# Kernel tuning notes

Measured on AMD Instinct MI355X. Metric: run time of the kernel, lower is better.

Reference implementation:

```python
import jax, jax.numpy as jnp
import numpy as np

D = 256; NH = 8; NL = 4; NP = 4; HD = D // NH
SHAPES = np.array([[64, 64], [32, 32], [16, 16], [8, 8]], dtype=np.int32)  # (H, W) per level
LSI = np.array([0, 4096, 5120, 5376], dtype=np.int32)
B = 4; LQ = int(SHAPES.prod(axis=1).sum())  # 5440


def setup_inputs() -> dict:
    key = jax.random.key(0)
    ks = jax.random.split(key, 16)
    p = lambda i, shape, s=0.02: jax.random.normal(ks[i], shape, dtype=jnp.float32) * s
    return dict(
        src=jax.random.normal(ks[0], (B, LQ, D), dtype=jnp.float32),
        pos=jax.random.normal(ks[1], (B, LQ, D), dtype=jnp.float32),
        reference_points=jax.random.uniform(ks[2], (B, LQ, NL, 2), dtype=jnp.float32),
        spatial_shapes=jnp.asarray(SHAPES),
        level_start_index=jnp.asarray(LSI),
        Wv=p(3, (D, D)), bv=jnp.zeros((D,), jnp.float32),
        Woff=p(4, (D, NH * NL * NP * 2)), boff=p(5, (NH * NL * NP * 2,)),
        Wattn=p(6, (D, NH * NL * NP)), battn=p(7, (NH * NL * NP,)),
        Wout=p(8, (D, D)), bout=jnp.zeros((D,), jnp.float32),
        g1=jnp.ones((D,), jnp.float32), b1=jnp.zeros((D,), jnp.float32),
        W1=p(9, (D, D)), bb1=jnp.zeros((D,), jnp.float32),
        W2=p(10, (D, D)), bb2=jnp.zeros((D,), jnp.float32),
        g3=jnp.ones((D,), jnp.float32), b3=jnp.zeros((D,), jnp.float32),
    )


def _ln(x, g, b, eps=1e-5):
    m = jnp.mean(x, -1, keepdims=True)
    v = jnp.mean(jnp.square(x - m), -1, keepdims=True)
    return (x - m) * jax.lax.rsqrt(v + eps) * g + b


def _bilinear(vflat, Hl, Wl, loc):
    # vflat: [B, Hl*Wl, nh, hd]; loc: [B, Lq, nh, np, 2] normalized to [0,1]
    # align_corners=False, zero padding (matches F.grid_sample in MSDeformAttn)
    x = loc[..., 0] * Wl - 0.5
    y = loc[..., 1] * Hl - 0.5
    x0 = jnp.floor(x); y0 = jnp.floor(y)
    fx = x - x0; fy = y - y0
    x0 = x0.astype(jnp.int32); y0 = y0.astype(jnp.int32)
    Bb, Lq, nh, npnt = x0.shape
    hd = vflat.shape[-1]
    out = jnp.zeros((Bb, Lq, nh, npnt, hd), vflat.dtype)
    for dy in (0, 1):
        for dx in (0, 1):
            xi = x0 + dx; yi = y0 + dy
            w = (fx if dx else 1.0 - fx) * (fy if dy else 1.0 - fy)
            valid = (xi >= 0) & (xi < Wl) & (yi >= 0) & (yi < Hl)
            idx = jnp.clip(yi, 0, Hl - 1) * Wl + jnp.clip(xi, 0, Wl - 1)  # [B,Lq,nh,np]
            idx = idx.transpose(0, 1, 3, 2).reshape(Bb, Lq * npnt, nh, 1)
            g = jnp.take_along_axis(vflat, idx, axis=1)
            g = g.reshape(Bb, Lq, npnt, nh, hd).transpose(0, 1, 3, 2, 4)
            out = out + g * (w * valid.astype(w.dtype))[..., None]
    return out  # [B, Lq, nh, np, hd]


def _forward(src, pos, reference_points, spatial_shapes, level_start_index,
             Wv, bv, Woff, boff, Wattn, battn, Wout, bout,
             g1, b1, W1, bb1, W2, bb2, g3, b3):
    shapes = np.asarray(spatial_shapes)
    lsi = np.asarray(level_start_index)
    Bq, Lq, Dm = src.shape
    q = src + pos  # with_pos_embed
    value = (src @ Wv + bv).reshape(Bq, Lq, NH, HD)
    off = (q @ Woff + boff).reshape(Bq, Lq, NH, NL, NP, 2)
    aw = jax.nn.softmax((q @ Wattn + battn).reshape(Bq, Lq, NH, NL * NP), axis=-1)
    aw = aw.reshape(Bq, Lq, NH, NL, NP)
    # offset normalizer is (W, H) per level
    norm = jnp.stack([shapes[:, 1].astype(np.float32), shapes[:, 0].astype(np.float32)], axis=-1)
    loc = reference_points[:, :, None, :, None, :] + off / norm[None, None, None, :, None, :]
    attended = jnp.zeros((Bq, Lq, NH, HD), src.dtype)
    for l in range(shapes.shape[0]):
        Hl, Wl = int(shapes[l, 0]), int(shapes[l, 1])
        s = int(lsi[l])
        vflat = value[:, s:s + Hl * Wl]
        sampled = _bilinear(vflat, Hl, Wl, loc[:, :, :, l])  # [B,Lq,nh,np,hd]
        attended = attended + jnp.einsum('blhpd,blhp->blhd', sampled, aw[:, :, :, l])
    src2 = attended.reshape(Bq, Lq, Dm) @ Wout + bout
    # residual + LayerNorm (dropout is identity in eval)
    sxy = _ln(src + src2, g1, b1)
    # FFN (d_ffn == d_model here), residual + LayerNorm
    h = jax.nn.relu(sxy @ W1 + bb1)
    return _ln(sxy + (h @ W2 + bb2), g3, b3)


def reference(src, pos, reference_points, spatial_shapes, level_start_index,
              Wv, bv, Woff, boff, Wattn, battn, Wout, bout,
              g1, b1, W1, bb1, W2, bb2, g3, b3):
    return _forward(src, pos, reference_points, spatial_shapes, level_start_index,
                    Wv, bv, Woff, boff, Wattn, battn, Wout, bout,
                    g1, b1, W1, bb1, W2, bb2, g3, b3)
```

## Files before the change

kernel.cpp:

```cpp
#include <hip/hip_runtime.h>
#include <cstddef>
#include <cstdint>

#define M_TOK 21760
#define LQ_ 5440

typedef _Float16 f16x8 __attribute__((ext_vector_type(8)));
typedef _Float16 h2v __attribute__((ext_vector_type(2)));
typedef float f32x4v __attribute__((ext_vector_type(4)));
typedef _Float16 half4v __attribute__((ext_vector_type(4)));

__device__ __forceinline__ unsigned short f2h(float f) {
  return __builtin_bit_cast(unsigned short, (_Float16)f);
}
__device__ __forceinline__ float h2f(unsigned short u) {
  return (float)__builtin_bit_cast(_Float16, u);
}

__global__ __launch_bounds__(256) void prep_k(
    const float* __restrict__ src, const float* __restrict__ pos,
    const float* __restrict__ Wv, const float* __restrict__ Woff,
    const float* __restrict__ Wattn, const float* __restrict__ Wout,
    const float* __restrict__ W1, const float* __restrict__ W2,
    unsigned short* __restrict__ s16, unsigned short* __restrict__ q16,
    unsigned short* __restrict__ G)
{
  const int b = blockIdx.x;
  if (b < 5440) {
    const int i = b * 256 + threadIdx.x;
    const float4 s = ((const float4*)src)[i];
    const float4 p = ((const float4*)pos)[i];
    ushort4 a, q;
    a.x = f2h(s.x); a.y = f2h(s.y); a.z = f2h(s.z); a.w = f2h(s.w);
    q.x = f2h(s.x + p.x); q.y = f2h(s.y + p.y); q.z = f2h(s.z + p.z); q.w = f2h(s.w + p.w);
    ((ushort4*)s16)[i] = a;
    ((ushort4*)q16)[i] = q;
  } else {
    const int gid = (b - 5440) * 256 + threadIdx.x;
    const float* srcs[6] = {Wv, Woff, Wattn, Wout, W1, W2};
    const int starts[7] = {0, 65536, 131072, 163840, 229376, 294912, 360448};
    const int Nn[6] = {256, 256, 128, 256, 256, 256};
    int m = 0;
#pragma unroll
    for (int i = 1; i < 6; ++i) m += (gid >= starts[i]);
    const int local = gid - starts[m];
    const int n = local >> 8;
    const int k = local & 255;
    G[gid] = f2h(srcs[m][(size_t)k * Nn[m] + n]);
  }
}

__global__ __launch_bounds__(256, 2) void gemm_qkv_k(
    const unsigned short* __restrict__ s16, const unsigned short* __restrict__ q16,
    const unsigned short* __restrict__ WvT, const unsigned short* __restrict__ WfT,
    const float* __restrict__ bv, const float* __restrict__ boff,
    const float* __restrict__ battn,
    unsigned short* __restrict__ value16, unsigned short* __restrict__ fused16)
{
  const int id = blockIdx.x;
  const int xcd = id & 7;
  const int local = id >> 3;
  const int sid = xcd * 106 + min(xcd, 2) + local;
  const int bx = sid / 5;
  const int by = sid % 5;

  const bool isv = (by < 2);
  const unsigned short* A  = isv ? s16 : q16;
  const unsigned short* Wt = isv ? WvT : WfT;
  const int n0 = isv ? by * 128 : (by - 2) * 128;
  const int N  = isv ? 256 : 384;
  unsigned short* out16 = isv ? value16 : fused16;
  const float* bsel; int nsub;
  if (isv)            { bsel = bv;    nsub = 0; }
  else if (n0 < 256)  { bsel = boff;  nsub = 0; }
  else                { bsel = battn; nsub = 256; }

  __shared__ unsigned short As[128 * 64];
  __shared__ unsigned short Bs[128 * 64];
  const int t = threadIdx.x;
  const int lane = t & 63, wave = t >> 6;
  const int wm = wave >> 1, wn = wave & 1;
  const int m0 = bx * 128;

  const int lrow = lane >> 3;
  const int pcol = (lane & 7) << 4;
  const int scol = pcol ^ (lrow << 4);

  f32x4v acc[4][4];
#pragma unroll
  for (int i = 0; i < 4; ++i)
#pragma unroll
    for (int j = 0; j < 4; ++j) acc[i][j] = (f32x4v){0.f, 0.f, 0.f, 0.f};

  const int fr = lane & 15;
  const int fkb = (lane >> 4) << 4;

  for (int k0 = 0; k0 < 256; k0 += 64) {
#pragma unroll
    for (int i = 0; i < 4; ++i) {
      const int row = wave * 32 + i * 8 + lrow;
      const unsigned short* g = A + (size_t)(m0 + row) * 256 + k0 + (scol >> 1);
      unsigned short* s = As + (wave * 32 + i * 8) * 64;
      __builtin_amdgcn_global_load_lds(
          (const __attribute__((address_space(1))) void*)g,
          (__attribute__((address_space(3))) void*)s, 16, 0, 0);
    }
#pragma unroll
    for (int i = 0; i < 4; ++i) {
      const int row = wave * 32 + i * 8 + lrow;
      const unsigned short* g = Wt + (size_t)(n0 + row) * 256 + k0 + (scol >> 1);
      unsigned short* s = Bs + (wave * 32 + i * 8) * 64;
      __builtin_amdgcn_global_load_lds(
          (const __attribute__((address_space(1))) void*)g,
          (__attribute__((address_space(3))) void*)s, 16, 0, 0);
    }
    __syncthreads();

    f16x8 af[4][2], bfr[4][2];
#pragma unroll
    for (int i = 0; i < 4; ++i) {
      const int row = wm * 64 + i * 16 + fr;
      const char* base = (const char*)As + row * 128;
#pragma unroll
      for (int kk = 0; kk < 2; ++kk)
        af[i][kk] = *(const f16x8*)(base + ((kk * 64 + fkb) ^ ((row & 7) << 4)));
    }
#pragma unroll
    for (int j = 0; j < 4; ++j) {
      const int row = wn * 64 + j * 16 + fr;
      const char* base = (const char*)Bs + row * 128;
#pragma unroll
      for (int kk = 0; kk < 2; ++kk)
        bfr[j][kk] = *(const f16x8*)(base + ((kk * 64 + fkb) ^ ((row & 7) << 4)));
    }
#pragma unroll
    for (int i = 0; i < 4; ++i)
#pragma unroll
      for (int j = 0; j < 4; ++j) {
        acc[i][j] = __builtin_amdgcn_mfma_f32_16x16x32_f16(af[i][0], bfr[j][0], acc[i][j], 0, 0, 0);
        acc[i][j] = __builtin_amdgcn_mfma_f32_16x16x32_f16(af[i][1], bfr[j][1], acc[i][j], 0, 0, 0);
      }
    __syncthreads();
  }

  const int fq = lane >> 4;
#pragma unroll
  for (int j = 0; j < 4; ++j) {
    const int n = n0 + wn * 64 + j * 16 + fr;
    const float bj = bsel[n - nsub];
#pragma unroll
    for (int i = 0; i < 4; ++i) {
#pragma unroll
      for (int r = 0; r < 4; ++r) {
        const int m = m0 + wm * 64 + i * 16 + fq * 4 + r;
        out16[(size_t)m * N + n] = f2h(acc[i][j][r] + bj);
      }
    }
  }
}

__global__ __launch_bounds__(512, 4) void gemm_ln_k(
    const unsigned short* __restrict__ A, const unsigned short* __restrict__ Wt,
    const float* __restrict__ bias, const float* __restrict__ resf,
    const unsigned short* __restrict__ res16,
    const float* __restrict__ g, const float* __restrict__ b,
    float* __restrict__ outf, unsigned short* __restrict__ out16)
{
  __shared__ unsigned short As[32 * 64];
  __shared__ unsigned short Bs[256 * 64 + 288];
  const int t = threadIdx.x;
  const int lane = t & 63, wave = t >> 6;
  const int rt = wave & 1, cg = wave >> 1;
  const int m0 = blockIdx.x * 32;

  const int lrow = lane >> 3;
  const int pcol = (lane & 7) << 4;
  const int scol = pcol ^ (lrow << 4);

  f32x4v acc[4];
#pragma unroll
  for (int j = 0; j < 4; ++j) acc[j] = (f32x4v){0.f, 0.f, 0.f, 0.f};

  const int fr = lane & 15;
  const int fq = lane >> 4;
  const int fkb = fq << 4;

  for (int k0 = 0; k0 < 256; k0 += 64) {
    if (wave < 4) {
      const int row = wave * 8 + lrow;
      const unsigned short* gp = A + (size_t)(m0 + row) * 256 + k0 + (scol >> 1);
      unsigned short* s = As + (wave * 8) * 64;
      __builtin_amdgcn_global_load_lds(
          (const __attribute__((address_space(1))) void*)gp,
          (__attribute__((address_space(3))) void*)s, 16, 0, 0);
    }
#pragma unroll
    for (int i = 0; i < 4; ++i) {
      const int row = wave * 32 + i * 8 + lrow;
      const unsigned short* gp = Wt + (size_t)row * 256 + k0 + (scol >> 1);
      unsigned short* s = Bs + (wave * 32 + i * 8) * 64;
      __builtin_amdgcn_global_load_lds(
          (const __attribute__((address_space(1))) void*)gp,
          (__attribute__((address_space(3))) void*)s, 16, 0, 0);
    }
    __syncthreads();

    f16x8 af0, af1;
    {
      const int arow = rt * 16 + fr;
      const char* abase = (const char*)As + arow * 128;
      af0 = *(const f16x8*)(abase + ((0 + fkb) ^ ((arow & 7) << 4)));
      af1 = *(const f16x8*)(abase + ((64 + fkb) ^ ((arow & 7) << 4)));
    }
#pragma unroll
    for (int j = 0; j < 4; ++j) {
      const int brow = cg * 64 + j * 16 + fr;
      const char* bbase = (const char*)Bs + brow * 128;
      const f16x8 b0 = *(const f16x8*)(bbase + ((0 + fkb) ^ ((brow & 7) << 4)));
      const f16x8 b1 = *(const f16x8*)(bbase + ((64 + fkb) ^ ((brow & 7) << 4)));
      acc[j] = __builtin_amdgcn_mfma_f32_16x16x32_f16(af0, b0, acc[j], 0, 0, 0);
      acc[j] = __builtin_amdgcn_mfma_f32_16x16x32_f16(af1, b1, acc[j], 0, 0, 0);
    }
    __syncthreads();
  }

  float* Cs = (float*)Bs;
#pragma unroll
  for (int j = 0; j < 4; ++j) {
    const int col = cg * 64 + j * 16 + fr;
#pragma unroll
    for (int rr = 0; rr < 4; ++rr) {
      const int row = rt * 16 + fq * 4 + rr;
      Cs[row * 260 + col] = acc[j][rr];
    }
  }
  __syncthreads();

  const int lg = lane >> 4, li = lane & 15;
  const int row = wave * 4 + lg;
  const size_t rowoff = (size_t)(m0 + row) * 256;

  float4 v[4];
  float s = 0.f;
#pragma unroll
  for (int c4 = 0; c4 < 4; ++c4) {
    const int col = c4 * 64 + li * 4;
    float4 x = *(float4*)&Cs[row * 260 + col];
    const float4 bi = *(const float4*)&bias[col];
    float4 rv;
    if (resf) {
      rv = *(const float4*)&resf[rowoff + col];
    } else {
      const ushort4 r16 = *(const ushort4*)&res16[rowoff + col];
      rv.x = h2f(r16.x); rv.y = h2f(r16.y); rv.z = h2f(r16.z); rv.w = h2f(r16.w);
    }
    x.x += bi.x + rv.x; x.y += bi.y + rv.y;
    x.z += bi.z + rv.z; x.w += bi.w + rv.w;
    v[c4] = x;
    s += x.x + x.y + x.z + x.w;
  }
#pragma unroll
  for (int o = 1; o < 16; o <<= 1) s += __shfl_xor(s, o);
  const float mean = s * (1.f / 256.f);
  float ss = 0.f;
#pragma unroll
  for (int c4 = 0; c4 < 4; ++c4) {
    const float d0 = v[c4].x - mean, d1 = v[c4].y - mean;
    const float d2 = v[c4].z - mean, d3 = v[c4].w - mean;
    ss += d0 * d0 + d1 * d1 + d2 * d2 + d3 * d3;
  }
#pragma unroll
  for (int o = 1; o < 16; o <<= 1) ss += __shfl_xor(ss, o);
  const float rstd = rsqrtf(ss * (1.f / 256.f) + 1e-5f);

#pragma unroll
  for (int c4 = 0; c4 < 4; ++c4) {
    const int col = c4 * 64 + li * 4;
    const float4 gv = *(const float4*)&g[col];
    const float4 bv = *(const float4*)&b[col];
    float4 o4;
    o4.x = (v[c4].x - mean) * rstd * gv.x + bv.x;
    o4.y = (v[c4].y - mean) * rstd * gv.y + bv.y;
    o4.z = (v[c4].z - mean) * rstd * gv.z + bv.z;
    o4.w = (v[c4].w - mean) * rstd * gv.w + bv.w;
    if (outf) *(float4*)(outf + rowoff + col) = o4;
    if (out16) {
      ushort4 o;
      o.x = f2h(o4.x); o.y = f2h(o4.y); o.z = f2h(o4.z); o.w = f2h(o4.w);
      *(ushort4*)(out16 + rowoff + col) = o;
    }
  }
}

__global__ __launch_bounds__(512, 4) void gemm_ffn_ln_k(
    const unsigned short* __restrict__ sxy16,
    const unsigned short* __restrict__ W1T, const unsigned short* __restrict__ W2T,
    const float* __restrict__ bb1, const float* __restrict__ bb2,
    const float* __restrict__ g, const float* __restrict__ b,
    float* __restrict__ outf)
{
  __shared__ unsigned short Bs[256 * 64 + 288];
  __shared__ unsigned short Hs[32 * 264];
  const int t = threadIdx.x;
  const int lane = t & 63, wave = t >> 6;
  const int rt = wave & 1, cg = wave >> 1;
  const int m0 = blockIdx.x * 32;

  const int lrow = lane >> 3;
  const int pcol = (lane & 7) << 4;
  const int scol = pcol ^ (lrow << 4);

  const int fr = lane & 15;
  const int fq = lane >> 4;
  const int fkb = fq << 4;

  f32x4v acc[4];
#pragma unroll
  for (int j = 0; j < 4; ++j) acc[j] = (f32x4v){0.f, 0.f, 0.f, 0.f};

  for (int k0 = 0; k0 < 256; k0 += 64) {
#pragma unroll
    for (int i = 0; i < 4; ++i) {
      const int row = wave * 32 + i * 8 + lrow;
      const unsigned short* gp = W1T + (size_t)row * 256 + k0 + (scol >> 1);
      unsigned short* s = Bs + (wave * 32 + i * 8) * 64;
      __builtin_amdgcn_global_load_lds(
          (const __attribute__((address_space(1))) void*)gp,
          (__attribute__((address_space(3))) void*)s, 16, 0, 0);
    }
    const unsigned short* ap = sxy16 + (size_t)(m0 + rt * 16 + fr) * 256 + k0 + fq * 8;
    const f16x8 af0 = *(const f16x8*)ap;
    const f16x8 af1 = *(const f16x8*)(ap + 32);
    __syncthreads();
#pragma unroll
    for (int j = 0; j < 4; ++j) {
      const int brow = cg * 64 + j * 16 + fr;
      const char* bbase = (const char*)Bs + brow * 128;
      const f16x8 b0 = *(const f16x8*)(bbase + ((0 + fkb) ^ ((brow & 7) << 4)));
      const f16x8 b1 = *(const f16x8*)(bbase + ((64 + fkb) ^ ((brow & 7) << 4)));
      acc[j] = __builtin_amdgcn_mfma_f32_16x16x32_f16(af0, b0, acc[j], 0, 0, 0);
      acc[j] = __builtin_amdgcn_mfma_f32_16x16x32_f16(af1, b1, acc[j], 0, 0, 0);
    }
    __syncthreads();
  }

  {
    float b1j[4];
#pragma unroll
    for (int j = 0; j < 4; ++j) b1j[j] = bb1[cg * 64 + j * 16 + fr];
#pragma unroll
    for (int j = 0; j < 4; ++j) {
      const int col = cg * 64 + j * 16 + fr;
#pragma unroll
      for (int rr = 0; rr < 4; ++rr) {
        const int row = rt * 16 + fq * 4 + rr;
        Hs[row * 264 + col] = f2h(fmaxf(acc[j][rr] + b1j[j], 0.f));
      }
      acc[j] = (f32x4v){0.f, 0.f, 0.f, 0.f};
    }
  }
  __syncthreads();

  for (int k0 = 0; k0 < 256; k0 += 64) {
#pragma unroll
    for (int i = 0; i < 4; ++i) {
      const int row = wave * 32 + i * 8 + lrow;
      const unsigned short* gp = W2T + (size_t)row * 256 + k0 + (scol >> 1);
      unsigned short* s = Bs + (wave * 32 + i * 8) * 64;
      __builtin_amdgcn_global_load_lds(
          (const __attribute__((address_space(1))) void*)gp,
          (__attribute__((address_space(3))) void*)s, 16, 0, 0);
    }
    const int arow = rt * 16 + fr;
    const f16x8 af0 = *(const f16x8*)&Hs[arow * 264 + k0 + fq * 8];
    const f16x8 af1 = *(const f16x8*)&Hs[arow * 264 + k0 + fq * 8 + 32];
    __syncthreads();
#pragma unroll
    for (int j = 0; j < 4; ++j) {
      const int brow = cg * 64 + j * 16 + fr;
      const char* bbase = (const char*)Bs + brow * 128;
      const f16x8 b0 = *(const f16x8*)(bbase + ((0 + fkb) ^ ((brow & 7) << 4)));
      const f16x8 b1 = *(const f16x8*)(bbase + ((64 + fkb) ^ ((brow & 7) << 4)));
      acc[j] = __builtin_amdgcn_mfma_f32_16x16x32_f16(af0, b0, acc[j], 0, 0, 0);
      acc[j] = __builtin_amdgcn_mfma_f32_16x16x32_f16(af1, b1, acc[j], 0, 0, 0);
    }
    __syncthreads();
  }

  float* Cs = (float*)Bs;
#pragma unroll
  for (int j = 0; j < 4; ++j) {
    const int col = cg * 64 + j * 16 + fr;
#pragma unroll
    for (int rr = 0; rr < 4; ++rr) {
      const int row = rt * 16 + fq * 4 + rr;
      Cs[row * 260 + col] = acc[j][rr];
    }
  }
  __syncthreads();

  const int lg = lane >> 4, li = lane & 15;
  const int row = wave * 4 + lg;
  const size_t rowoff = (size_t)(m0 + row) * 256;

  float4 v[4];
  float s = 0.f;
#pragma unroll
  for (int c4 = 0; c4 < 4; ++c4) {
    const int col = c4 * 64 + li * 4;
    float4 x = *(float4*)&Cs[row * 260 + col];
    const float4 bi = *(const float4*)&bb2[col];
    const ushort4 r16 = *(const ushort4*)&sxy16[rowoff + col];
    x.x += bi.x + h2f(r16.x); x.y += bi.y + h2f(r16.y);
    x.z += bi.z + h2f(r16.z); x.w += bi.w + h2f(r16.w);
    v[c4] = x;
    s += x.x + x.y + x.z + x.w;
  }
#pragma unroll
  for (int o = 1; o < 16; o <<= 1) s += __shfl_xor(s, o);
  const float mean = s * (1.f / 256.f);
  float ss = 0.f;
#pragma unroll
  for (int c4 = 0; c4 < 4; ++c4) {
    const float d0 = v[c4].x - mean, d1 = v[c4].y - mean;
    const float d2 = v[c4].z - mean, d3 = v[c4].w - mean;
    ss += d0 * d0 + d1 * d1 + d2 * d2 + d3 * d3;
  }
#pragma unroll
  for (int o = 1; o < 16; o <<= 1) ss += __shfl_xor(ss, o);
  const float rstd = rsqrtf(ss * (1.f / 256.f) + 1e-5f);

#pragma unroll
  for (int c4 = 0; c4 < 4; ++c4) {
    const int col = c4 * 64 + li * 4;
    const float4 gv = *(const float4*)&g[col];
    const float4 bv = *(const float4*)&b[col];
    float4 o4;
    o4.x = (v[c4].x - mean) * rstd * gv.x + bv.x;
    o4.y = (v[c4].y - mean) * rstd * gv.y + bv.y;
    o4.z = (v[c4].z - mean) * rstd * gv.z + bv.z;
    o4.w = (v[c4].w - mean) * rstd * gv.w + bv.w;
    *(float4*)(outf + rowoff + col) = o4;
  }
}

__global__ __launch_bounds__(256) void samp_k(
    const unsigned short* __restrict__ value16, const unsigned short* __restrict__ fused16,
    const float* __restrict__ ref, unsigned short* __restrict__ att16)
{
  const int b = blockIdx.x;
  const int wg = (b & 7) * 340 + (b >> 3);
  const int tok0 = wg * 8;

  __shared__ half4v swv[8][136];
  __shared__ uint2  siv[8][136];
  const int t = threadIdx.x;
  const _Float16* fh = (const _Float16*)fused16;

#pragma unroll
  for (int it = 0; it < 4; ++it) {
    const int idx = it * 256 + t;
    const int ti = idx >> 7;
    const int e  = idx & 127;
    const int tok = tok0 + ti;
    const int h = e >> 4;
    const int lvl = (e >> 2) & 3;
    const int HW[4] = {64, 32, 16, 8};
    const int LS[4] = {0, 4096, 5120, 5376};
    const int Wl = HW[lvl];

    const float lg = (float)fh[(size_t)tok * 384 + 256 + e];
    float mx = lg;
#pragma unroll
    for (int o = 1; o < 16; o <<= 1) mx = fmaxf(mx, __shfl_xor(mx, o, 16));
    const float ex = __expf(lg - mx);
    float sm = ex;
#pragma unroll
    for (int o = 1; o < 16; o <<= 1) sm += __shfl_xor(sm, o, 16);
    const float a = ex / sm;

    const float ox = (float)fh[(size_t)tok * 384 + e * 2 + 0];
    const float oy = (float)fh[(size_t)tok * 384 + e * 2 + 1];
    const float rx = ref[(size_t)tok * 8 + lvl * 2 + 0];
    const float ry = ref[(size_t)tok * 8 + lvl * 2 + 1];
    const float x = rx * (float)Wl + ox - 0.5f;
    const float y = ry * (float)Wl + oy - 0.5f;
    const float x0f = floorf(x), y0f = floorf(y);
    const float fx = x - x0f, fy = y - y0f;
    const int x0 = (int)x0f, y0 = (int)y0f;

    const int xi1 = x0 + 1, yi1 = y0 + 1;
    const float wx0 = 1.f - fx, wx1 = fx, wy0 = 1.f - fy, wy1 = fy;
    const int xc0 = min(max(x0, 0), Wl - 1), xc1 = min(max(xi1, 0), Wl - 1);
    const int yc0 = min(max(y0, 0), Wl - 1), yc1 = min(max(yi1, 0), Wl - 1);
    const bool vx0 = (x0 >= 0) & (x0 < Wl), vx1 = (xi1 >= 0) & (xi1 < Wl);
    const bool vy0 = (y0 >= 0) & (y0 < Wl), vy1 = (yi1 >= 0) & (yi1 < Wl);
    half4v hw;
    hw.x = (_Float16)((vx0 & vy0) ? a * wx0 * wy0 : 0.f);
    hw.y = (_Float16)((vx1 & vy0) ? a * wx1 * wy0 : 0.f);
    hw.z = (_Float16)((vx0 & vy1) ? a * wx0 * wy1 : 0.f);
    hw.w = (_Float16)((vx1 & vy1) ? a * wx1 * wy1 : 0.f);
    const unsigned i00 = (unsigned)(LS[lvl] + yc0 * Wl + xc0);
    const unsigned i01 = (unsigned)(LS[lvl] + yc0 * Wl + xc1);
    const unsigned i10 = (unsigned)(LS[lvl] + yc1 * Wl + xc0);
    const unsigned i11 = (unsigned)(LS[lvl] + yc1 * Wl + xc1);
    uint2 io;
    io.x = i00 | (i01 << 16);
    io.y = i10 | (i11 << 16);
    const int sl = e + h;
    swv[ti][sl] = hw;
    siv[ti][sl] = io;
  }
  __syncthreads();

  const int wave = t >> 6, lane = t & 63;
  const int ti = wave * 2 + (lane >> 5);
  const int h = (lane >> 2) & 7, dg = lane & 3;
  const int tok = tok0 + ti;
  const int vbase = (tok0 / LQ_) * LQ_;
  const char* vb = (const char*)(value16 + (size_t)vbase * 256);
  const int laneoff = h * 64 + dg * 16;
  h2v a0 = {0, 0}, a1 = {0, 0}, a2 = {0, 0}, a3 = {0, 0};
  const int ebase = h * 17;

#pragma unroll 4
  for (int p = 0; p < 16; ++p) {
    const half4v hw = swv[ti][ebase + p];
    const uint2 io = siv[ti][ebase + p];
    const int o00 = (int)((io.x & 0xFFFFu) << 9) + laneoff;
    const int o01 = (int)((io.x >> 16) << 9) + laneoff;
    const int o10 = (int)((io.y & 0xFFFFu) << 9) + laneoff;
    const int o11 = (int)((io.y >> 16) << 9) + laneoff;
    const uint4 u0 = *(const uint4*)(vb + o00);
    const uint4 u1 = *(const uint4*)(vb + o01);
    const uint4 u2 = *(const uint4*)(vb + o10);
    const uint4 u3 = *(const uint4*)(vb + o11);
#define CORNER(U, WI) {                                            \
    const h2v w2 = __builtin_shufflevector(hw, hw, WI, WI);        \
    a0 += w2 * __builtin_bit_cast(h2v, U.x);                       \
    a1 += w2 * __builtin_bit_cast(h2v, U.y);                       \
    a2 += w2 * __builtin_bit_cast(h2v, U.z);                       \
    a3 += w2 * __builtin_bit_cast(h2v, U.w); }
    CORNER(u0, 0) CORNER(u1, 1) CORNER(u2, 2) CORNER(u3, 3)
#undef CORNER
  }

  uint4 o;
  o.x = __builtin_bit_cast(unsigned, a0);
  o.y = __builtin_bit_cast(unsigned, a1);
  o.z = __builtin_bit_cast(unsigned, a2);
  o.w = __builtin_bit_cast(unsigned, a3);
  *(uint4*)(att16 + (size_t)tok * 256 + h * 32 + dg * 8) = o;
}

extern "C" void kernel_launch(void* const* d_in, const int* in_sizes, int n_in,
                              void* d_out, int out_size, void* d_ws, size_t ws_size,
                              hipStream_t stream)
{
  const float* src   = (const float*)d_in[0];
  const float* pos   = (const float*)d_in[1];
  const float* ref   = (const float*)d_in[2];
  const float* Wv    = (const float*)d_in[5];
  const float* bv    = (const float*)d_in[6];
  const float* Woff  = (const float*)d_in[7];
  const float* boff  = (const float*)d_in[8];
  const float* Wattn = (const float*)d_in[9];
  const float* battn = (const float*)d_in[10];
  const float* Wout  = (const float*)d_in[11];
  const float* bout  = (const float*)d_in[12];
  const float* g1    = (const float*)d_in[13];
  const float* b1    = (const float*)d_in[14];
  const float* W1    = (const float*)d_in[15];
  const float* bb1   = (const float*)d_in[16];
  const float* W2    = (const float*)d_in[17];
  const float* bb2   = (const float*)d_in[18];
  const float* g3    = (const float*)d_in[19];
  const float* b3    = (const float*)d_in[20];

  float* out = (float*)d_out;
  char* ws = (char*)d_ws;
  const size_t M = M_TOK;

  unsigned short* value16 = (unsigned short*)ws;
  unsigned short* fused16 = (unsigned short*)(ws + M * 256 * 4);
  unsigned short* bufE = fused16 + M * 384;
  unsigned short* bufF = bufE + M * 256;
  unsigned short* bufG = bufF + M * 256;

  unsigned short* WvT     = bufG + 0;
  unsigned short* WfusedT = bufG + 65536;
  unsigned short* WoutT   = bufG + 163840;
  unsigned short* W1T     = bufG + 229376;
  unsigned short* W2T     = bufG + 294912;

  const dim3 blk(256);

  prep_k<<<dim3(6848), blk, 0, stream>>>(src, pos, Wv, Woff, Wattn, Wout, W1, W2,
                                         bufE, bufF, bufG);
  gemm_qkv_k<<<dim3(850), blk, 0, stream>>>(bufE, bufF, WvT, WfusedT,
                                            bv, boff, battn, value16, fused16);
  samp_k<<<dim3(2720), blk, 0, stream>>>(value16, fused16, ref, bufE);
  gemm_ln_k<<<dim3(680), dim3(512), 0, stream>>>(bufE, WoutT, bout, src, nullptr,
                                                 g1, b1, nullptr, bufF);
  gemm_ffn_ln_k<<<dim3(680), dim3(512), 0, stream>>>(bufF, W1T, W2T, bb1, bb2,
                                                     g3, b3, out);
}
```

Before: 99.54 us.

## Fuse deformable sampling into output-projection GEMM + LayerNorm kernel

Merges the bilinear sampling kernel into the Wout GEMM + residual + LayerNorm kernel. Each 512-thread block samples 32 tokens in two passes of 16, writing the attended rows directly into an LDS A-tile, then runs the GEMM from LDS. The sampling LDS tables share a region with the B tile and the C staging buffer. This removes one launch and the global round trip of the attended activations, at the cost of more LDS per block and 680 blocks for the sampling phase instead of 2720 smaller ones.

```diff
diff --git a/kernel.cpp b/kernel.cpp
--- a/kernel.cpp
+++ b/kernel.cpp
@@ -159,41 +159,139 @@
   }
 }
 
-__global__ __launch_bounds__(512, 4) void gemm_ln_k(
-    const unsigned short* __restrict__ A, const unsigned short* __restrict__ Wt,
+__global__ __launch_bounds__(512, 4) void samp_ln_k(
+    const unsigned short* __restrict__ value16, const unsigned short* __restrict__ fused16,
+    const float* __restrict__ ref, const unsigned short* __restrict__ Wt,
     const float* __restrict__ bias, const float* __restrict__ resf,
-    const unsigned short* __restrict__ res16,
     const float* __restrict__ g, const float* __restrict__ b,
-    float* __restrict__ outf, unsigned short* __restrict__ out16)
+    unsigned short* __restrict__ out16)
 {
-  __shared__ unsigned short As[32 * 64];
-  __shared__ unsigned short Bs[256 * 64 + 288];
+  const int bid = blockIdx.x;
+  const int wg = (bid & 7) * 85 + (bid >> 3);
+  const int tok0 = wg * 32;
+
+  __shared__ unsigned short As[32 * 264];
+  __shared__ __align__(16) unsigned char region2[34816];
+  half4v (*swv)[136] = (half4v(*)[136])region2;
+  uint2  (*siv)[136] = (uint2 (*)[136])(region2 + 17408);
+  unsigned short* Bs = (unsigned short*)region2;
+  float* Cs = (float*)region2;
+
   const int t = threadIdx.x;
   const int lane = t & 63, wave = t >> 6;
+  const _Float16* fh = (const _Float16*)fused16;
+  const int vbase = (tok0 / LQ_) * LQ_;
+  const char* vb = (const char*)(value16 + (size_t)vbase * 256);
+
+#pragma unroll 1
+  for (int sp = 0; sp < 2; ++sp) {
+#pragma unroll
+    for (int it = 0; it < 4; ++it) {
+      const int idx = it * 512 + t;
+      const int ti = idx >> 7;
+      const int e  = idx & 127;
+      const int tok = tok0 + sp * 16 + ti;
+      const int h = e >> 4;
+      const int lvl = (e >> 2) & 3;
+      const int HW[4] = {64, 32, 16, 8};
+      const int LS[4] = {0, 4096, 5120, 5376};
+      const int Wl = HW[lvl];
+
+      const float lg = (float)fh[(size_t)tok * 384 + 256 + e];
+      float mx = lg;
+#pragma unroll
+      for (int o = 1; o < 16; o <<= 1) mx = fmaxf(mx, __shfl_xor(mx, o, 16));
+      const float ex = __expf(lg - mx);
+      float sm = ex;
+#pragma unroll
+      for (int o = 1; o < 16; o <<= 1) sm += __shfl_xor(sm, o, 16);
+      const float a = ex / sm;
+
+      const float ox = (float)fh[(size_t)tok * 384 + e * 2 + 0];
+      const float oy = (float)fh[(size_t)tok * 384 + e * 2 + 1];
+      const float rx = ref[(size_t)tok * 8 + lvl * 2 + 0];
+      const float ry = ref[(size_t)tok * 8 + lvl * 2 + 1];
+      const float x = rx * (float)Wl + ox - 0.5f;
+      const float y = ry * (float)Wl + oy - 0.5f;
+      const float x0f = floorf(x), y0f = floorf(y);
+      const float fx = x - x0f, fy = y - y0f;
+      const int x0 = (int)x0f, y0 = (int)y0f;
+
+      const int xi1 = x0 + 1, yi1 = y0 + 1;
+      const float wx0 = 1.f - fx, wx1 = fx, wy0 = 1.f - fy, wy1 = fy;
+      const int xc0 = min(max(x0, 0), Wl - 1), xc1 = min(max(xi1, 0), Wl - 1);
+      const int yc0 = min(max(y0, 0), Wl - 1), yc1 = min(max(yi1, 0), Wl - 1);
+      const bool vx0 = (x0 >= 0) & (x0 < Wl), vx1 = (xi1 >= 0) & (xi1 < Wl);
+      const bool vy0 = (y0 >= 0) & (y0 < Wl), vy1 = (yi1 >= 0) & (yi1 < Wl);
+      half4v hw;
+      hw.x = (_Float16)((vx0 & vy0) ? a * wx0 * wy0 : 0.f);
+      hw.y = (_Float16)((vx1 & vy0) ? a * wx1 * wy0 : 0.f);
+      hw.z = (_Float16)((vx0 & vy1) ? a * wx0 * wy1 : 0.f);
+      hw.w = (_Float16)((vx1 & vy1) ? a * wx1 * wy1 : 0.f);
+      const unsigned i00 = (unsigned)(LS[lvl] + yc0 * Wl + xc0);
+      const unsigned i01 = (unsigned)(LS[lvl] + yc0 * Wl + xc1);
+      const unsigned i10 = (unsigned)(LS[lvl] + yc1 * Wl + xc0);
+      const unsigned i11 = (unsigned)(LS[lvl] + yc1 * Wl + xc1);
+      uint2 io;
+      io.x = i00 | (i01 << 16);
+      io.y = i10 | (i11 << 16);
+      const int sl = e + h;
+      swv[ti][sl] = hw;
+      siv[ti][sl] = io;
+    }
+    __syncthreads();
+
+    {
+      const int ti = wave * 2 + (lane >> 5);
+      const int h = (lane >> 2) & 7, dg = lane & 3;
+      const int laneoff = h * 64 + dg * 16;
+      h2v a0 = {0, 0}, a1 = {0, 0}, a2 = {0, 0}, a3 = {0, 0};
+      const int ebase = h * 17;
+
+#pragma unroll 4
+      for (int p = 0; p < 16; ++p) {
+        const half4v hw = swv[ti][ebase + p];
+        const uint2 io = siv[ti][ebase + p];
+        const int o00 = (int)((io.x & 0xFFFFu) << 9) + laneoff;
+        const int o01 = (int)((io.x >> 16) << 9) + laneoff;
+        const int o10 = (int)((io.y & 0xFFFFu) << 9) + laneoff;
+        const int o11 = (int)((io.y >> 16) << 9) + laneoff;
+        const uint4 u0 = *(const uint4*)(vb + o00);
+        const uint4 u1 = *(const uint4*)(vb + o01);
+        const uint4 u2 = *(const uint4*)(vb + o10);
+        const uint4 u3 = *(const uint4*)(vb + o11);
+#define CORNER(U, WI) {                                            \
+        const h2v w2 = __builtin_shufflevector(hw, hw, WI, WI);    \
+        a0 += w2 * __builtin_bit_cast(h2v, U.x);                   \
+        a1 += w2 * __builtin_bit_cast(h2v, U.y);                   \
+        a2 += w2 * __builtin_bit_cast(h2v, U.z);                   \
+        a3 += w2 * __builtin_bit_cast(h2v, U.w); }
+        CORNER(u0, 0) CORNER(u1, 1) CORNER(u2, 2) CORNER(u3, 3)
+#undef CORNER
+      }
+      uint4 o;
+      o.x = __builtin_bit_cast(unsigned, a0);
+      o.y = __builtin_bit_cast(unsigned, a1);
+      o.z = __builtin_bit_cast(unsigned, a2);
+      o.w = __builtin_bit_cast(unsigned, a3);
+      *(uint4*)&As[(sp * 16 + ti) * 264 + h * 32 + dg * 8] = o;
+    }
+    __syncthreads();
+  }
+
   const int rt = wave & 1, cg = wave >> 1;
-  const int m0 = blockIdx.x * 32;
-
   const int lrow = lane >> 3;
   const int pcol = (lane & 7) << 4;
   const int scol = pcol ^ (lrow << 4);
-
-  f32x4v acc[4];
-#pragma unroll
-  for (int j = 0; j < 4; ++j) acc[j] = (f32x4v){0.f, 0.f, 0.f, 0.f};
-
   const int fr = lane & 15;
   const int fq = lane >> 4;
   const int fkb = fq << 4;
 
+  f32x4v acc[4];
+#pragma unroll
+  for (int j = 0; j < 4; ++j) acc[j] = (f32x4v){0.f, 0.f, 0.f, 0.f};
+
   for (int k0 = 0; k0 < 256; k0 += 64) {
-    if (wave < 4) {
-      const int row = wave * 8 + lrow;
-      const unsigned short* gp = A + (size_t)(m0 + row) * 256 + k0 + (scol >> 1);
-      unsigned short* s = As + (wave * 8) * 64;
-      __builtin_amdgcn_global_load_lds(
-          (const __attribute__((address_space(1))) void*)gp,
-          (__attribute__((address_space(3))) void*)s, 16, 0, 0);
-    }
 #pragma unroll
     for (int i = 0; i < 4; ++i) {
       const int row = wave * 32 + i * 8 + lrow;
@@ -203,15 +301,10 @@
           (const __attribute__((address_space(1))) void*)gp,
           (__attribute__((address_space(3))) void*)s, 16, 0, 0);
     }
-    __syncthreads();
-
-    f16x8 af0, af1;
-    {
-      const int arow = rt * 16 + fr;
-      const char* abase = (const char*)As + arow * 128;
-      af0 = *(const f16x8*)(abase + ((0 + fkb) ^ ((arow & 7) << 4)));
-      af1 = *(const f16x8*)(abase + ((64 + fkb) ^ ((arow & 7) << 4)));
-    }
+    const int arow = rt * 16 + fr;
+    const f16x8 af0 = *(const f16x8*)&As[arow * 264 + k0 + fq * 8];
+    const f16x8 af1 = *(const f16x8*)&As[arow * 264 + k0 + fq * 8 + 32];
+    __syncthreads();
 #pragma unroll
     for (int j = 0; j < 4; ++j) {
       const int brow = cg * 64 + j * 16 + fr;
@@ -224,7 +317,6 @@
     __syncthreads();
   }
 
-  float* Cs = (float*)Bs;
 #pragma unroll
   for (int j = 0; j < 4; ++j) {
     const int col = cg * 64 + j * 16 + fr;
@@ -238,7 +330,7 @@
 
   const int lg = lane >> 4, li = lane & 15;
   const int row = wave * 4 + lg;
-  const size_t rowoff = (size_t)(m0 + row) * 256;
+  const size_t rowoff = (size_t)(tok0 + row) * 256;
 
   float4 v[4];
   float s = 0.f;
@@ -247,13 +339,7 @@
     const int col = c4 * 64 + li * 4;
     float4 x = *(float4*)&Cs[row * 260 + col];
     const float4 bi = *(const float4*)&bias[col];
-    float4 rv;
-    if (resf) {
-      rv = *(const float4*)&resf[rowoff + col];
-    } else {
-      const ushort4 r16 = *(const ushort4*)&res16[rowoff + col];
-      rv.x = h2f(r16.x); rv.y = h2f(r16.y); rv.z = h2f(r16.z); rv.w = h2f(r16.w);
-    }
+    const float4 rv = *(const float4*)&resf[rowoff + col];
     x.x += bi.x + rv.x; x.y += bi.y + rv.y;
     x.z += bi.z + rv.z; x.w += bi.w + rv.w;
     v[c4] = x;
@@ -278,17 +364,12 @@
     const int col = c4 * 64 + li * 4;
     const float4 gv = *(const float4*)&g[col];
     const float4 bv = *(const float4*)&b[col];
-    float4 o4;
-    o4.x = (v[c4].x - mean) * rstd * gv.x + bv.x;
-    o4.y = (v[c4].y - mean) * rstd * gv.y + bv.y;
-    o4.z = (v[c4].z - mean) * rstd * gv.z + bv.z;
-    o4.w = (v[c4].w - mean) * rstd * gv.w + bv.w;
-    if (outf) *(float4*)(outf + rowoff + col) = o4;
-    if (out16) {
-      ushort4 o;
-      o.x = f2h(o4.x); o.y = f2h(o4.y); o.z = f2h(o4.z); o.w = f2h(o4.w);
-      *(ushort4*)(out16 + rowoff + col) = o;
-    }
+    ushort4 o;
+    o.x = f2h((v[c4].x - mean) * rstd * gv.x + bv.x);
+    o.y = f2h((v[c4].y - mean) * rstd * gv.y + bv.y);
+    o.z = f2h((v[c4].z - mean) * rstd * gv.z + bv.z);
+    o.w = f2h((v[c4].w - mean) * rstd * gv.w + bv.w);
+    *(ushort4*)(out16 + rowoff + col) = o;
   }
 }
 
@@ -442,115 +523,6 @@
     o4.w = (v[c4].w - mean) * rstd * gv.w + bv.w;
     *(float4*)(outf + rowoff + col) = o4;
   }
-}
-
-__global__ __launch_bounds__(256) void samp_k(
-    const unsigned short* __restrict__ value16, const unsigned short* __restrict__ fused16,
-    const float* __restrict__ ref, unsigned short* __restrict__ att16)
-{
-  const int b = blockIdx.x;
-  const int wg = (b & 7) * 340 + (b >> 3);
-  const int tok0 = wg * 8;
-
-  __shared__ half4v swv[8][136];
-  __shared__ uint2  siv[8][136];
-  const int t = threadIdx.x;
-  const _Float16* fh = (const _Float16*)fused16;
-
-#pragma unroll
-  for (int it = 0; it < 4; ++it) {
-    const int idx = it * 256 + t;
-    const int ti = idx >> 7;
-    const int e  = idx & 127;
-    const int tok = tok0 + ti;
-    const int h = e >> 4;
-    const int lvl = (e >> 2) & 3;
-    const int HW[4] = {64, 32, 16, 8};
-    const int LS[4] = {0, 4096, 5120, 5376};
-    const int Wl = HW[lvl];
-
-    const float lg = (float)fh[(size_t)tok * 384 + 256 + e];
-    float mx = lg;
-#pragma unroll
-    for (int o = 1; o < 16; o <<= 1) mx = fmaxf(mx, __shfl_xor(mx, o, 16));
-    const float ex = __expf(lg - mx);
-    float sm = ex;
-#pragma unroll
-    for (int o = 1; o < 16; o <<= 1) sm += __shfl_xor(sm, o, 16);
-    const float a = ex / sm;
-
-    const float ox = (float)fh[(size_t)tok * 384 + e * 2 + 0];
-    const float oy = (float)fh[(size_t)tok * 384 + e * 2 + 1];
-    const float rx = ref[(size_t)tok * 8 + lvl * 2 + 0];
-    const float ry = ref[(size_t)tok * 8 + lvl * 2 + 1];
-    const float x = rx * (float)Wl + ox - 0.5f;
-    const float y = ry * (float)Wl + oy - 0.5f;
-    const float x0f = floorf(x), y0f = floorf(y);
-    const float fx = x - x0f, fy = y - y0f;
-    const int x0 = (int)x0f, y0 = (int)y0f;
-
-    const int xi1 = x0 + 1, yi1 = y0 + 1;
-    const float wx0 = 1.f - fx, wx1 = fx, wy0 = 1.f - fy, wy1 = fy;
-    const int xc0 = min(max(x0, 0), Wl - 1), xc1 = min(max(xi1, 0), Wl - 1);
-    const int yc0 = min(max(y0, 0), Wl - 1), yc1 = min(max(yi1, 0), Wl - 1);
-    const bool vx0 = (x0 >= 0) & (x0 < Wl), vx1 = (xi1 >= 0) & (xi1 < Wl);
-    const bool vy0 = (y0 >= 0) & (y0 < Wl), vy1 = (yi1 >= 0) & (yi1 < Wl);
-    half4v hw;
-    hw.x = (_Float16)((vx0 & vy0) ? a * wx0 * wy0 : 0.f);
-    hw.y = (_Float16)((vx1 & vy0) ? a * wx1 * wy0 : 0.f);
-    hw.z = (_Float16)((vx0 & vy1) ? a * wx0 * wy1 : 0.f);
-    hw.w = (_Float16)((vx1 & vy1) ? a * wx1 * wy1 : 0.f);
-    const unsigned i00 = (unsigned)(LS[lvl] + yc0 * Wl + xc0);
-    const unsigned i01 = (unsigned)(LS[lvl] + yc0 * Wl + xc1);
-    const unsigned i10 = (unsigned)(LS[lvl] + yc1 * Wl + xc0);
-    const unsigned i11 = (unsigned)(LS[lvl] + yc1 * Wl + xc1);
-    uint2 io;
-    io.x = i00 | (i01 << 16);
-    io.y = i10 | (i11 << 16);
-    const int sl = e + h;
-    swv[ti][sl] = hw;
-    siv[ti][sl] = io;
-  }
-  __syncthreads();
-
-  const int wave = t >> 6, lane = t & 63;
-  const int ti = wave * 2 + (lane >> 5);
-  const int h = (lane >> 2) & 7, dg = lane & 3;
-  const int tok = tok0 + ti;
-  const int vbase = (tok0 / LQ_) * LQ_;
-  const char* vb = (const char*)(value16 + (size_t)vbase * 256);
-  const int laneoff = h * 64 + dg * 16;
-  h2v a0 = {0, 0}, a1 = {0, 0}, a2 = {0, 0}, a3 = {0, 0};
-  const int ebase = h * 17;
-
-#pragma unroll 4
-  for (int p = 0; p < 16; ++p) {
-    const half4v hw = swv[ti][ebase + p];
-    const uint2 io = siv[ti][ebase + p];
-    const int o00 = (int)((io.x & 0xFFFFu) << 9) + laneoff;
-    const int o01 = (int)((io.x >> 16) << 9) + laneoff;
-    const int o10 = (int)((io.y & 0xFFFFu) << 9) + laneoff;
-    const int o11 = (int)((io.y >> 16) << 9) + laneoff;
-    const uint4 u0 = *(const uint4*)(vb + o00);
-    const uint4 u1 = *(const uint4*)(vb + o01);
-    const uint4 u2 = *(const uint4*)(vb + o10);
-    const uint4 u3 = *(const uint4*)(vb + o11);
-#define CORNER(U, WI) {                                            \
-    const h2v w2 = __builtin_shufflevector(hw, hw, WI, WI);        \
-    a0 += w2 * __builtin_bit_cast(h2v, U.x);                       \
-    a1 += w2 * __builtin_bit_cast(h2v, U.y);                       \
-    a2 += w2 * __builtin_bit_cast(h2v, U.z);                       \
-    a3 += w2 * __builtin_bit_cast(h2v, U.w); }
-    CORNER(u0, 0) CORNER(u1, 1) CORNER(u2, 2) CORNER(u3, 3)
-#undef CORNER
-  }
-
-  uint4 o;
-  o.x = __builtin_bit_cast(unsigned, a0);
-  o.y = __builtin_bit_cast(unsigned, a1);
-  o.z = __builtin_bit_cast(unsigned, a2);
-  o.w = __builtin_bit_cast(unsigned, a3);
-  *(uint4*)(att16 + (size_t)tok * 256 + h * 32 + dg * 8) = o;
 }
 
 extern "C" void kernel_launch(void* const* d_in, const int* in_sizes, int n_in,
@@ -599,9 +571,8 @@
                                          bufE, bufF, bufG);
   gemm_qkv_k<<<dim3(850), blk, 0, stream>>>(bufE, bufF, WvT, WfusedT,
                                             bv, boff, battn, value16, fused16);
-  samp_k<<<dim3(2720), blk, 0, stream>>>(value16, fused16, ref, bufE);
-  gemm_ln_k<<<dim3(680), dim3(512), 0, stream>>>(bufE, WoutT, bout, src, nullptr,
-                                                 g1, b1, nullptr, bufF);
+  samp_ln_k<<<dim3(680), dim3(512), 0, stream>>>(value16, fused16, ref, WoutT,
+                                                 bout, src, g1, b1, bufF);
   gemm_ffn_ln_k<<<dim3(680), dim3(512), 0, stream>>>(bufF, W1T, W2T, bb1, bb2,
                                                      g3, b3, out);
 }
```

New measurement: 103.4 us. 3.8% more time.
